# Kernel tuning notes

Hardware: AMD Instinct MI355X
Metric: run time of the kernel (lower is better)

## Reference

```python
import jax, jax.numpy as jnp
import numpy as np

B = 8          # number of subgraphs (seq_start_end rows)
N = 2048       # nodes per subgraph (equal-size segments)
D = 64         # h_dim
H = 4          # gat_heads
ALPHA = 0.2    # leaky relu slope


def setup_inputs() -> dict:
    key = jax.random.key(0)
    k1, k2, k3, k4, k5 = jax.random.split(key, 5)
    h_states = jax.random.normal(k1, (B * N, D), dtype=jnp.float32)
    # xavier-ish scales
    W_heads = jax.random.normal(k2, (H, D, D), dtype=jnp.float32) * (1.414 * np.sqrt(2.0 / (D + D)))
    a_heads = jax.random.normal(k3, (H, 2 * D), dtype=jnp.float32) * (1.414 * np.sqrt(2.0 / (2 * D + 1)))
    W_out = jax.random.normal(k4, (H * D, D), dtype=jnp.float32) * (1.414 * np.sqrt(2.0 / (H * D + D)))
    a_out = jax.random.normal(k5, (2 * D,), dtype=jnp.float32) * (1.414 * np.sqrt(2.0 / (2 * D + 1)))
    starts = jnp.arange(B, dtype=jnp.int32) * N
    seq_start_end = jnp.stack([starts, starts + N], axis=1)  # (B, 2)
    return {"h_states": h_states, "W_heads": W_heads, "a_heads": a_heads,
            "W_out": W_out, "a_out": a_out, "seq_start_end": seq_start_end}


def _gat_layer(x, W, a):
    """Dense GAT layer. Equivalent to the torch.cat O(N^2*2d) construction,
    rewritten as separate a1/a2 projections + broadcast add. Eval mode (no dropout)."""
    h = x @ W                      # (N, dout)
    d = W.shape[1]
    s1 = h @ a[:d]                 # (N,)  score contribution of source node i
    s2 = h @ a[d:]                 # (N,)  score contribution of target node j
    e = jax.nn.leaky_relu(s1[:, None] + s2[None, :], ALPHA)  # (N, N)
    attn = jax.nn.softmax(e, axis=1)
    return attn @ h                # (N, dout)


def reference(h_states, W_heads, a_heads, W_out, a_out, seq_start_end):
    # seq_start_end encodes B equal contiguous segments of length N -> reshape
    x = h_states.reshape(B, N, D)

    def per_graph(xg):  # xg: (N, D)
        # multi-head attention layers, concat=True -> elu on each head output
        hp = jax.vmap(lambda W, a: jax.nn.elu(_gat_layer(xg, W, a)))(W_heads, a_heads)  # (H, N, D)
        xc = jnp.transpose(hp, (1, 0, 2)).reshape(N, H * D)
        # output attention layer, concat=False (no elu inside), then elu + log_softmax outside
        out = jax.nn.elu(_gat_layer(xc, W_out, a_out))   # (N, D)
        return jax.nn.log_softmax(out, axis=1)

    return jax.vmap(per_graph)(x).reshape(B * N, D)
```

## Files before the change

kernel.cpp:

```cpp
#include <hip/hip_runtime.h>
#include <math.h>

#define NTOT 16384
#define NSEG 2048
#define TROW 65
#define TSTRIDE 133185ull

#define OFF_HH   0ull
#define OFF_XC   4194304ull
#define OFF_S1H  8388608ull
#define OFF_S2H  8454144ull
#define OFF_S1O  8519680ull
#define OFF_S2O  8536064ull
#define OFF_SVAL 8552448ull
#define OFF_WN   8617984ull
#define OFF_CHA  8683520ull
#define OFF_CHS  8949760ull
#define OFF_SIDX 9216000ull
#define OFF_A    9281536ull
#define OFF_S    13543456ull

__device__ inline unsigned long long pack_key(float v, int idx) {
    unsigned u = __float_as_uint(v);
    u = (u & 0x80000000u) ? ~u : (u | 0x80000000u);
    return ((unsigned long long)u << 32) | (unsigned)idx;
}
__device__ inline float unpack_key(unsigned long long k) {
    unsigned u = (unsigned)(k >> 32);
    u = (u & 0x80000000u) ? (u ^ 0x80000000u) : ~u;
    return __uint_as_float(u);
}
__device__ inline unsigned long long shfl_xor_u64(unsigned long long x, int mask) {
    unsigned lo = (unsigned)x, hi = (unsigned)(x >> 32);
    lo = (unsigned)__shfl_xor((int)lo, mask, 64);
    hi = (unsigned)__shfl_xor((int)hi, mask, 64);
    return ((unsigned long long)hi << 32) | lo;
}

__global__ __launch_bounds__(256) void gemm1_k(const float* __restrict__ X,
                                               const float* __restrict__ Wh,
                                               const float* __restrict__ aH,
                                               float* __restrict__ hh,
                                               float* __restrict__ s1h,
                                               float* __restrict__ s2h) {
    __shared__ float As[64][68];
    __shared__ float Bs[64][68];
    const int tid = threadIdx.x;
    const int bm = blockIdx.x, h = blockIdx.y;
    const int c0 = tid & 63, r0 = tid >> 6;
#pragma unroll
    for (int r = 0; r < 16; ++r) {
        int row = r0 + r * 4;
        As[c0][row] = X[(size_t)(bm * 64 + row) * 64 + c0];
        Bs[row][c0] = Wh[h * 4096 + row * 64 + c0];
    }
    __syncthreads();
    const int tx = tid & 15, ty = tid >> 4;
    const int m0 = ty * 4, n0 = tx * 4;
    float acc[4][4] = {};
#pragma unroll
    for (int kk = 0; kk < 64; ++kk) {
        float4 a = *(const float4*)&As[kk][m0];
        float4 b = *(const float4*)&Bs[kk][n0];
        acc[0][0] += a.x * b.x; acc[0][1] += a.x * b.y; acc[0][2] += a.x * b.z; acc[0][3] += a.x * b.w;
        acc[1][0] += a.y * b.x; acc[1][1] += a.y * b.y; acc[1][2] += a.y * b.z; acc[1][3] += a.y * b.w;
        acc[2][0] += a.z * b.x; acc[2][1] += a.z * b.y; acc[2][2] += a.z * b.z; acc[2][3] += a.z * b.w;
        acc[3][0] += a.w * b.x; acc[3][1] += a.w * b.y; acc[3][2] += a.w * b.z; acc[3][3] += a.w * b.w;
    }
#pragma unroll
    for (int i = 0; i < 4; ++i) {
        float4 v = make_float4(acc[i][0], acc[i][1], acc[i][2], acc[i][3]);
        *(float4*)&hh[(size_t)(bm * 64 + m0 + i) * 256 + h * 64 + n0] = v;
    }
#pragma unroll
    for (int i = 0; i < 4; ++i) {
        float p1 = 0.f, p2 = 0.f;
#pragma unroll
        for (int jj = 0; jj < 4; ++jj) {
            p1 += acc[i][jj] * aH[h * 128 + n0 + jj];
            p2 += acc[i][jj] * aH[h * 128 + 64 + n0 + jj];
        }
#pragma unroll
        for (int off = 8; off; off >>= 1) {
            p1 += __shfl_xor(p1, off, 16);
            p2 += __shfl_xor(p2, off, 16);
        }
        if (tx == 0) {
            s1h[h * NTOT + bm * 64 + m0 + i] = p1;
            s2h[h * NTOT + bm * 64 + m0 + i] = p2;
        }
    }
}

__global__ __launch_bounds__(256) void gemm2_k(const float* __restrict__ XC,
                                               const float* __restrict__ Wo,
                                               const float* __restrict__ aO,
                                               float* __restrict__ hc,
                                               float* __restrict__ s1o,
                                               float* __restrict__ s2o) {
    __shared__ float As[64][68];
    __shared__ float Bs[64][68];
    const int tid = threadIdx.x;
    const int bm = blockIdx.x;
    const int c0 = tid & 63, r0 = tid >> 6;
    const int tx = tid & 15, ty = tid >> 4;
    const int m0 = ty * 4, n0 = tx * 4;
    float acc[4][4] = {};
    for (int kt = 0; kt < 4; ++kt) {
#pragma unroll
        for (int r = 0; r < 16; ++r) {
            int row = r0 + r * 4;
            As[c0][row] = XC[(size_t)(bm * 64 + row) * 256 + kt * 64 + c0];
            Bs[row][c0] = Wo[(kt * 64 + row) * 64 + c0];
        }
        __syncthreads();
#pragma unroll
        for (int kk = 0; kk < 64; ++kk) {
            float4 a = *(const float4*)&As[kk][m0];
            float4 b = *(const float4*)&Bs[kk][n0];
            acc[0][0] += a.x * b.x; acc[0][1] += a.x * b.y; acc[0][2] += a.x * b.z; acc[0][3] += a.x * b.w;
            acc[1][0] += a.y * b.x; acc[1][1] += a.y * b.y; acc[1][2] += a.y * b.z; acc[1][3] += a.y * b.w;
            acc[2][0] += a.z * b.x; acc[2][1] += a.z * b.y; acc[2][2] += a.z * b.z; acc[2][3] += a.z * b.w;
            acc[3][0] += a.w * b.x; acc[3][1] += a.w * b.y; acc[3][2] += a.w * b.z; acc[3][3] += a.w * b.w;
        }
        __syncthreads();
    }
#pragma unroll
    for (int i = 0; i < 4; ++i) {
        float4 v = make_float4(acc[i][0], acc[i][1], acc[i][2], acc[i][3]);
        *(float4*)&hc[(size_t)(bm * 64 + m0 + i) * 64 + n0] = v;
    }
#pragma unroll
    for (int i = 0; i < 4; ++i) {
        float p1 = 0.f, p2 = 0.f;
#pragma unroll
        for (int jj = 0; jj < 4; ++jj) {
            p1 += acc[i][jj] * aO[n0 + jj];
            p2 += acc[i][jj] * aO[64 + n0 + jj];
        }
#pragma unroll
        for (int off = 8; off; off >>= 1) {
            p1 += __shfl_xor(p1, off, 16);
            p2 += __shfl_xor(p2, off, 16);
        }
        if (tx == 0) {
            s1o[bm * 64 + m0 + i] = p1;
            s2o[bm * 64 + m0 + i] = p2;
        }
    }
}

__global__ __launch_bounds__(1024) void sortchunkscan_k(const float* __restrict__ s2_all,
                                                        const float* __restrict__ V,
                                                        int heads, int vstride,
                                                        float* __restrict__ g_sval, int* __restrict__ g_sidx,
                                                        float* __restrict__ g_wN,
                                                        float* __restrict__ g_chA, float* __restrict__ g_chS,
                                                        float* __restrict__ g_A, float* __restrict__ g_S) {
    __shared__ unsigned long long sA[1024];
    __shared__ unsigned long long sB[1024];
    __shared__ float chA[8320];
    __shared__ float chS[8320];
    __shared__ float swn[NSEG];
    __shared__ int ssi[NSEG];
    __shared__ float btA[4][65];
    __shared__ float btS[4][65];
    __shared__ float sM2;
    const int tid = threadIdx.x, t = blockIdx.x;
    const int g = t / heads, h = t % heads;
    const float* s2p = s2_all + (size_t)h * NTOT + (size_t)g * NSEG;
    const float* Vp = V + (size_t)g * NSEG * vstride + h * 64;

    unsigned long long a0 = pack_key(s2p[tid], tid);
    unsigned long long a1 = pack_key(s2p[tid + 1024], tid + 1024);
    for (int k = 2; k <= 2048; k <<= 1) {
        const bool up0 = (tid & k) == 0;
        const bool up1 = (((tid + 1024) & k) == 0);
        for (int j = k >> 1; j > 0; j >>= 1) {
            if (j >= 1024) {
                unsigned long long lo = a0 < a1 ? a0 : a1;
                unsigned long long hi = a0 < a1 ? a1 : a0;
                a0 = up0 ? lo : hi;
                a1 = up0 ? hi : lo;
            } else if (j >= 64) {
                __syncthreads();
                sA[tid] = a0; sB[tid] = a1;
                __syncthreads();
                unsigned long long p0 = sA[tid ^ j], p1 = sB[tid ^ j];
                bool lower = (tid & j) == 0;
                a0 = ((a0 < p0) == (lower == up0)) ? a0 : p0;
                a1 = ((a1 < p1) == (lower == up1)) ? a1 : p1;
            } else {
                unsigned long long p0 = shfl_xor_u64(a0, j);
                unsigned long long p1 = shfl_xor_u64(a1, j);
                bool lower = (tid & j) == 0;
                a0 = ((a0 < p0) == (lower == up0)) ? a0 : p0;
                a1 = ((a1 < p1) == (lower == up1)) ? a1 : p1;
            }
        }
    }
    float v0 = unpack_key(a0), v1 = unpack_key(a1);
    if (tid == 1023) sM2 = v1;
    __syncthreads();
    const float M2 = sM2;
    int i0 = (int)(unsigned)(a0 & 0xffffffffu);
    int i1 = (int)(unsigned)(a1 & 0xffffffffu);
    float w0 = __expf(0.2f * (v0 - M2));
    float w1 = __expf(0.2f * (v1 - M2));
    size_t o = (size_t)t * NSEG;
    g_sval[o + tid] = v0; g_sval[o + tid + 1024] = v1;
    g_sidx[o + tid] = i0; g_sidx[o + tid + 1024] = i1;
    g_wN[o + tid] = w0;   g_wN[o + tid + 1024] = w1;
    swn[tid] = w0; swn[tid + 1024] = w1;
    ssi[tid] = i0; ssi[tid + 1024] = i1;
    __syncthreads();
    const int wv = tid >> 6, lane = tid & 63;
    for (int cc = 0; cc < 8; ++cc) {
        int c = wv * 8 + cc, base = c * 16;
        float sa = 0.f, swa = 0.f, ss = 0.f, sws = 0.f;
#pragma unroll
        for (int j = 0; j < 16; ++j) {
            float wn = swn[base + j];
            int row = ssi[base + j];
            float v = Vp[(size_t)row * vstride + lane];
            float w2 = wn * wn, wp = w2 * w2 * wn;
            sa += wn * v; swa += wn;
            ss += wp * v; sws += wp;
        }
        chA[c * 65 + lane] = sa; chS[c * 65 + lane] = ss;
        if (lane == 0) { chA[c * 65 + 64] = swa; chS[c * 65 + 64] = sws; }
    }
    __syncthreads();
    if (tid < 260) {
        int b = tid / 65, d = tid % 65;
        float run = 0.f;
        for (int c = b * 32; c < b * 32 + 32; ++c) { float v = chA[c * 65 + d]; chA[c * 65 + d] = run; run += v; }
        btA[b][d] = run;
    } else if (tid >= 512 && tid < 772) {
        int u = tid - 512;
        int b = u / 65, d = u % 65;
        float run = 0.f;
        for (int c = b * 32 + 31; c >= b * 32; --c) { run += chS[c * 65 + d]; chS[c * 65 + d] = run; }
        btS[b][d] = run;
    }
    __syncthreads();
    if (tid < 65) {
        float run = 0.f;
        for (int b = 0; b < 4; ++b) { float v = btA[b][tid]; btA[b][tid] = run; run += v; }
        g_A[(size_t)t * TSTRIDE + (size_t)2048 * TROW + tid] = run;
    } else if (tid >= 512 && tid < 577) {
        int d = tid - 512;
        float run = 0.f;
        for (int b = 3; b >= 0; --b) { float v = btS[b][d]; btS[b][d] = run; run += v; }
        g_S[(size_t)t * TSTRIDE + (size_t)2048 * TROW + d] = 0.f;
    }
    __syncthreads();
    if (tid < 512) {
        for (int i = tid; i < 8320; i += 512) chA[i] += btA[(i / 65) >> 5][i % 65];
    } else {
        for (int i = tid - 512; i < 8320; i += 512) chS[i] += btS[(i / 65) >> 5][i % 65];
    }
    __syncthreads();
    for (int i = tid; i < 8320; i += 1024) {
        g_chA[(size_t)t * 8320 + i] = chA[i];
        g_chS[(size_t)t * 8320 + i] = chS[i];
    }
}

__global__ __launch_bounds__(256) void seg_tab_k(const float* __restrict__ V,
                                                 int heads, int vstride,
                                                 const int* __restrict__ g_sidx,
                                                 const float* __restrict__ g_wN,
                                                 const float* __restrict__ g_chA,
                                                 const float* __restrict__ g_chS,
                                                 float* __restrict__ g_A, float* __restrict__ g_S) {
    const int t = blockIdx.y, g = t / heads, h = t % heads;
    const int wv = threadIdx.x >> 6, lane = threadIdx.x & 63;
    const int c = blockIdx.x * 4 + wv;
    const int base = c * 16;
    const float* Vp = V + (size_t)g * NSEG * vstride + h * 64;
    const int* sidx = g_sidx + (size_t)t * NSEG + base;
    const float* wnp = g_wN + (size_t)t * NSEG + base;
    float wn[16], vv[16];
#pragma unroll
    for (int j = 0; j < 16; ++j) wn[j] = wnp[j];
#pragma unroll
    for (int j = 0; j < 16; ++j) vv[j] = Vp[(size_t)sidx[j] * vstride + lane];
    float* A = g_A + (size_t)t * TSTRIDE;
    float* S = g_S + (size_t)t * TSTRIDE;
    float accA = g_chA[((size_t)t * 128 + c) * TROW + lane];
    float scaA = g_chA[((size_t)t * 128 + c) * TROW + 64];
#pragma unroll
    for (int j = 0; j < 16; ++j) {
        size_t pos = base + j;
        A[pos * TROW + lane] = accA;
        if (lane == 0) A[pos * TROW + 64] = scaA;
        accA += wn[j] * vv[j]; scaA += wn[j];
    }
    float accS = 0.f, scaS = 0.f;
    if (c < 127) {
        accS = g_chS[((size_t)t * 128 + c + 1) * TROW + lane];
        scaS = g_chS[((size_t)t * 128 + c + 1) * TROW + 64];
    }
#pragma unroll
    for (int j = 15; j >= 0; --j) {
        float w = wn[j], w2 = w * w, wp = w2 * w2 * w;
        accS += wp * vv[j]; scaS += wp;
        size_t pos = base + j;
        S[pos * TROW + lane] = accS;
        if (lane == 0) S[pos * TROW + 64] = scaS;
    }
}

template <int MODE>
__global__ __launch_bounds__(256) void seg_query_k(const float* __restrict__ s1_all,
                                                   float* __restrict__ out,
                                                   int heads, int ostride,
                                                   const float* __restrict__ g_sval,
                                                   const float* __restrict__ g_A,
                                                   const float* __restrict__ g_S) {
    __shared__ float sval[NSEG];
    const int tid = threadIdx.x;
    const int t = blockIdx.y, g = t / heads, h = t % heads;
    const float4* sv4 = (const float4*)(g_sval + (size_t)t * NSEG);
    for (int i = tid; i < NSEG / 4; i += 256) ((float4*)sval)[i] = sv4[i];
    __syncthreads();
    const float M2 = sval[NSEG - 1];
    const int lane = tid & 63, wv = tid >> 6;
    const int q0 = blockIdx.x * 64 + wv * 16;
    const float* s1p = s1_all + (size_t)h * NTOT + (size_t)g * NSEG;
    float* outp = out + (size_t)g * NSEG * ostride + h * 64;
    const float* A = g_A + (size_t)t * TSTRIDE;
    const float* S = g_S + (size_t)t * TSTRIDE;
    int myq = q0 + (lane & 15);
    float s1v = s1p[myq];
    float th = -s1v;
    int lo = 0, hi = NSEG;
    while (lo < hi) { int mid = (lo + hi) >> 1; if (sval[mid] <= th) lo = mid + 1; else hi = mid; }
    for (int j = 0; j < 16; ++j) {
        int k = __shfl(lo, j, 64);
        float s1q = __shfl(s1v, j, 64);
        const float* rowA = A + (size_t)k * TROW;
        const float* rowS = S + (size_t)k * TROW;
        float accA = rowA[lane], scaA = rowA[64];
        float accS = rowS[lane], scaS = rowS[64];
        float cc = __expf(-0.8f * fmaxf(s1q + M2, 0.f));
        float o = (accS + cc * accA) / (scaS + cc * scaA);
        o = o > 0.f ? o : expm1f(o);
        int q = q0 + j;
        if (MODE == 0) {
            outp[(size_t)q * ostride + lane] = o;
        } else {
            float m = o;
#pragma unroll
            for (int off = 32; off; off >>= 1) m = fmaxf(m, __shfl_xor(m, off, 64));
            float e = __expf(o - m);
#pragma unroll
            for (int off = 32; off; off >>= 1) e += __shfl_xor(e, off, 64);
            outp[(size_t)q * ostride + lane] = o - m - __logf(e);
        }
    }
}

extern "C" void kernel_launch(void* const* d_in, const int* in_sizes, int n_in,
                              void* d_out, int out_size, void* d_ws, size_t ws_size,
                              hipStream_t stream) {
    const float* h_states = (const float*)d_in[0];
    const float* W_heads = (const float*)d_in[1];
    const float* a_heads = (const float*)d_in[2];
    const float* W_out = (const float*)d_in[3];
    const float* a_out = (const float*)d_in[4];
    float* w = (float*)d_ws;
    float* hh = w + OFF_HH;
    float* xc = w + OFF_XC;
    float* hc = w + OFF_HH;
    float* s1h = w + OFF_S1H;
    float* s2h = w + OFF_S2H;
    float* s1o = w + OFF_S1O;
    float* s2o = w + OFF_S2O;
    float* g_sval = w + OFF_SVAL;
    float* g_wN = w + OFF_WN;
    float* g_chA = w + OFF_CHA;
    float* g_chS = w + OFF_CHS;
    int* g_sidx = (int*)(w + OFF_SIDX);
    float* g_A = w + OFF_A;
    float* g_S = w + OFF_S;
    float* outp = (float*)d_out;

    gemm1_k<<<dim3(256, 4), 256, 0, stream>>>(h_states, W_heads, a_heads, hh, s1h, s2h);
    sortchunkscan_k<<<32, 1024, 0, stream>>>(s2h, hh, 4, 256, g_sval, g_sidx, g_wN, g_chA, g_chS, g_A, g_S);
    seg_tab_k<<<dim3(32, 32), 256, 0, stream>>>(hh, 4, 256, g_sidx, g_wN, g_chA, g_chS, g_A, g_S);
    seg_query_k<0><<<dim3(32, 32), 256, 0, stream>>>(s1h, xc, 4, 256, g_sval, g_A, g_S);
    gemm2_k<<<256, 256, 0, stream>>>(xc, W_out, a_out, hc, s1o, s2o);
    sortchunkscan_k<<<8, 1024, 0, stream>>>(s2o, hc, 1, 64, g_sval, g_sidx, g_wN, g_chA, g_chS, g_A, g_S);
    seg_tab_k<<<dim3(32, 8), 256, 0, stream>>>(hc, 1, 64, g_sidx, g_wN, g_chA, g_chS, g_A, g_S);
    seg_query_k<1><<<dim3(32, 8), 256, 0, stream>>>(s1o, outp, 1, 64, g_sval, g_A, g_S);
}
```

Before: 203.6 us.

## Split sort from chunk scan and apply chunk prefixes at query time

The sort kernel no longer gathers V rows or computes chunk totals; it only sorts and writes sorted values, indices and weights. The table kernel now builds local within-chunk prefix and suffix sums plus per-chunk totals. A small new scan kernel computes the chunk-level exclusive prefixes, and the query kernel adds them when reading table rows. The bitonic sort also double-buffers its shared arrays to drop one barrier per step. This removes the heavy serial gather-and-scan from a 32-block kernel, at the cost of an extra launch and extra loads per query.

```diff
diff --git a/kernel.cpp b/kernel.cpp
--- a/kernel.cpp
+++ b/kernel.cpp
@@ -4,7 +4,8 @@
 #define NTOT 16384
 #define NSEG 2048
 #define TROW 65
-#define TSTRIDE 133185ull
+#define TSTRIDE 133120ull
+#define CSTRIDE 8385ull
 
 #define OFF_HH   0ull
 #define OFF_XC   4194304ull
@@ -14,11 +15,11 @@
 #define OFF_S2O  8536064ull
 #define OFF_SVAL 8552448ull
 #define OFF_WN   8617984ull
-#define OFF_CHA  8683520ull
-#define OFF_CHS  8949760ull
-#define OFF_SIDX 9216000ull
-#define OFF_A    9281536ull
-#define OFF_S    13543456ull
+#define OFF_SIDX 8683520ull
+#define OFF_CA   8749056ull
+#define OFF_CS   9017376ull
+#define OFF_A    9285696ull
+#define OFF_S    13545536ull
 
 __device__ inline unsigned long long pack_key(float v, int idx) {
     unsigned u = __float_as_uint(v);
@@ -150,29 +151,21 @@
     }
 }
 
-__global__ __launch_bounds__(1024) void sortchunkscan_k(const float* __restrict__ s2_all,
-                                                        const float* __restrict__ V,
-                                                        int heads, int vstride,
-                                                        float* __restrict__ g_sval, int* __restrict__ g_sidx,
-                                                        float* __restrict__ g_wN,
-                                                        float* __restrict__ g_chA, float* __restrict__ g_chS,
-                                                        float* __restrict__ g_A, float* __restrict__ g_S) {
-    __shared__ unsigned long long sA[1024];
-    __shared__ unsigned long long sB[1024];
-    __shared__ float chA[8320];
-    __shared__ float chS[8320];
-    __shared__ float swn[NSEG];
-    __shared__ int ssi[NSEG];
-    __shared__ float btA[4][65];
-    __shared__ float btS[4][65];
+__global__ __launch_bounds__(1024) void sort_k(const float* __restrict__ s2_all,
+                                               int heads,
+                                               float* __restrict__ g_sval,
+                                               int* __restrict__ g_sidx,
+                                               float* __restrict__ g_wN) {
+    __shared__ unsigned long long sA[2][1024];
+    __shared__ unsigned long long sB[2][1024];
     __shared__ float sM2;
     const int tid = threadIdx.x, t = blockIdx.x;
     const int g = t / heads, h = t % heads;
     const float* s2p = s2_all + (size_t)h * NTOT + (size_t)g * NSEG;
-    const float* Vp = V + (size_t)g * NSEG * vstride + h * 64;
 
     unsigned long long a0 = pack_key(s2p[tid], tid);
     unsigned long long a1 = pack_key(s2p[tid + 1024], tid + 1024);
+    int p = 0;
     for (int k = 2; k <= 2048; k <<= 1) {
         const bool up0 = (tid & k) == 0;
         const bool up1 = (((tid + 1024) & k) == 0);
@@ -183,19 +176,19 @@
                 a0 = up0 ? lo : hi;
                 a1 = up0 ? hi : lo;
             } else if (j >= 64) {
+                sA[p][tid] = a0; sB[p][tid] = a1;
                 __syncthreads();
-                sA[tid] = a0; sB[tid] = a1;
-                __syncthreads();
-                unsigned long long p0 = sA[tid ^ j], p1 = sB[tid ^ j];
+                unsigned long long q0 = sA[p][tid ^ j], q1 = sB[p][tid ^ j];
                 bool lower = (tid & j) == 0;
-                a0 = ((a0 < p0) == (lower == up0)) ? a0 : p0;
-                a1 = ((a1 < p1) == (lower == up1)) ? a1 : p1;
+                a0 = ((a0 < q0) == (lower == up0)) ? a0 : q0;
+                a1 = ((a1 < q1) == (lower == up1)) ? a1 : q1;
+                p ^= 1;
             } else {
-                unsigned long long p0 = shfl_xor_u64(a0, j);
-                unsigned long long p1 = shfl_xor_u64(a1, j);
+                unsigned long long q0 = shfl_xor_u64(a0, j);
+                unsigned long long q1 = shfl_xor_u64(a1, j);
                 bool lower = (tid & j) == 0;
-                a0 = ((a0 < p0) == (lower == up0)) ? a0 : p0;
-                a1 = ((a1 < p1) == (lower == up1)) ? a1 : p1;
+                a0 = ((a0 < q0) == (lower == up0)) ? a0 : q0;
+                a1 = ((a1 < q1) == (lower == up1)) ? a1 : q1;
             }
         }
     }
@@ -211,69 +204,14 @@
     g_sval[o + tid] = v0; g_sval[o + tid + 1024] = v1;
     g_sidx[o + tid] = i0; g_sidx[o + tid + 1024] = i1;
     g_wN[o + tid] = w0;   g_wN[o + tid + 1024] = w1;
-    swn[tid] = w0; swn[tid + 1024] = w1;
-    ssi[tid] = i0; ssi[tid + 1024] = i1;
-    __syncthreads();
-    const int wv = tid >> 6, lane = tid & 63;
-    for (int cc = 0; cc < 8; ++cc) {
-        int c = wv * 8 + cc, base = c * 16;
-        float sa = 0.f, swa = 0.f, ss = 0.f, sws = 0.f;
-#pragma unroll
-        for (int j = 0; j < 16; ++j) {
-            float wn = swn[base + j];
-            int row = ssi[base + j];
-            float v = Vp[(size_t)row * vstride + lane];
-            float w2 = wn * wn, wp = w2 * w2 * wn;
-            sa += wn * v; swa += wn;
-            ss += wp * v; sws += wp;
-        }
-        chA[c * 65 + lane] = sa; chS[c * 65 + lane] = ss;
-        if (lane == 0) { chA[c * 65 + 64] = swa; chS[c * 65 + 64] = sws; }
-    }
-    __syncthreads();
-    if (tid < 260) {
-        int b = tid / 65, d = tid % 65;
-        float run = 0.f;
-        for (int c = b * 32; c < b * 32 + 32; ++c) { float v = chA[c * 65 + d]; chA[c * 65 + d] = run; run += v; }
-        btA[b][d] = run;
-    } else if (tid >= 512 && tid < 772) {
-        int u = tid - 512;
-        int b = u / 65, d = u % 65;
-        float run = 0.f;
-        for (int c = b * 32 + 31; c >= b * 32; --c) { run += chS[c * 65 + d]; chS[c * 65 + d] = run; }
-        btS[b][d] = run;
-    }
-    __syncthreads();
-    if (tid < 65) {
-        float run = 0.f;
-        for (int b = 0; b < 4; ++b) { float v = btA[b][tid]; btA[b][tid] = run; run += v; }
-        g_A[(size_t)t * TSTRIDE + (size_t)2048 * TROW + tid] = run;
-    } else if (tid >= 512 && tid < 577) {
-        int d = tid - 512;
-        float run = 0.f;
-        for (int b = 3; b >= 0; --b) { float v = btS[b][d]; btS[b][d] = run; run += v; }
-        g_S[(size_t)t * TSTRIDE + (size_t)2048 * TROW + d] = 0.f;
-    }
-    __syncthreads();
-    if (tid < 512) {
-        for (int i = tid; i < 8320; i += 512) chA[i] += btA[(i / 65) >> 5][i % 65];
-    } else {
-        for (int i = tid - 512; i < 8320; i += 512) chS[i] += btS[(i / 65) >> 5][i % 65];
-    }
-    __syncthreads();
-    for (int i = tid; i < 8320; i += 1024) {
-        g_chA[(size_t)t * 8320 + i] = chA[i];
-        g_chS[(size_t)t * 8320 + i] = chS[i];
-    }
-}
-
-__global__ __launch_bounds__(256) void seg_tab_k(const float* __restrict__ V,
-                                                 int heads, int vstride,
-                                                 const int* __restrict__ g_sidx,
-                                                 const float* __restrict__ g_wN,
-                                                 const float* __restrict__ g_chA,
-                                                 const float* __restrict__ g_chS,
-                                                 float* __restrict__ g_A, float* __restrict__ g_S) {
+}
+
+__global__ __launch_bounds__(256) void tabw_k(const float* __restrict__ V,
+                                              int heads, int vstride,
+                                              const int* __restrict__ g_sidx,
+                                              const float* __restrict__ g_wN,
+                                              float* __restrict__ g_A, float* __restrict__ g_S,
+                                              float* __restrict__ g_TA, float* __restrict__ g_TS) {
     const int t = blockIdx.y, g = t / heads, h = t % heads;
     const int wv = threadIdx.x >> 6, lane = threadIdx.x & 63;
     const int c = blockIdx.x * 4 + wv;
@@ -288,8 +226,7 @@
     for (int j = 0; j < 16; ++j) vv[j] = Vp[(size_t)sidx[j] * vstride + lane];
     float* A = g_A + (size_t)t * TSTRIDE;
     float* S = g_S + (size_t)t * TSTRIDE;
-    float accA = g_chA[((size_t)t * 128 + c) * TROW + lane];
-    float scaA = g_chA[((size_t)t * 128 + c) * TROW + 64];
+    float accA = 0.f, scaA = 0.f;
 #pragma unroll
     for (int j = 0; j < 16; ++j) {
         size_t pos = base + j;
@@ -297,11 +234,9 @@
         if (lane == 0) A[pos * TROW + 64] = scaA;
         accA += wn[j] * vv[j]; scaA += wn[j];
     }
+    g_TA[((size_t)t * 128 + c) * TROW + lane] = accA;
+    if (lane == 0) g_TA[((size_t)t * 128 + c) * TROW + 64] = scaA;
     float accS = 0.f, scaS = 0.f;
-    if (c < 127) {
-        accS = g_chS[((size_t)t * 128 + c + 1) * TROW + lane];
-        scaS = g_chS[((size_t)t * 128 + c + 1) * TROW + 64];
-    }
 #pragma unroll
     for (int j = 15; j >= 0; --j) {
         float w = wn[j], w2 = w * w, wp = w2 * w2 * w;
@@ -310,15 +245,41 @@
         S[pos * TROW + lane] = accS;
         if (lane == 0) S[pos * TROW + 64] = scaS;
     }
+    g_TS[((size_t)t * 128 + c) * TROW + lane] = accS;
+    if (lane == 0) g_TS[((size_t)t * 128 + c) * TROW + 64] = scaS;
+}
+
+__global__ __launch_bounds__(256) void scan_k(const float* __restrict__ g_TA,
+                                              const float* __restrict__ g_TS,
+                                              float* __restrict__ g_CA,
+                                              float* __restrict__ g_CS) {
+    const int t = blockIdx.x, tid = threadIdx.x;
+    if (tid < 65) {
+        const float* TA = g_TA + (size_t)t * 128 * TROW + tid;
+        float* CA = g_CA + (size_t)t * CSTRIDE + tid;
+        float run = 0.f;
+#pragma unroll 4
+        for (int c = 0; c < 128; ++c) { CA[c * TROW] = run; run += TA[c * TROW]; }
+        CA[128 * TROW] = run;
+    } else if (tid >= 128 && tid < 193) {
+        const int d = tid - 128;
+        const float* TS = g_TS + (size_t)t * 128 * TROW + d;
+        float* CS = g_CS + (size_t)t * CSTRIDE + d;
+        float run = 0.f;
+#pragma unroll 4
+        for (int c = 127; c >= 0; --c) { CS[c * TROW] = run; run += TS[c * TROW]; }
+    }
 }
 
 template <int MODE>
-__global__ __launch_bounds__(256) void seg_query_k(const float* __restrict__ s1_all,
-                                                   float* __restrict__ out,
-                                                   int heads, int ostride,
-                                                   const float* __restrict__ g_sval,
-                                                   const float* __restrict__ g_A,
-                                                   const float* __restrict__ g_S) {
+__global__ __launch_bounds__(256) void query_k(const float* __restrict__ s1_all,
+                                               float* __restrict__ out,
+                                               int heads, int ostride,
+                                               const float* __restrict__ g_sval,
+                                               const float* __restrict__ g_A,
+                                               const float* __restrict__ g_S,
+                                               const float* __restrict__ g_CA,
+                                               const float* __restrict__ g_CS) {
     __shared__ float sval[NSEG];
     const int tid = threadIdx.x;
     const int t = blockIdx.y, g = t / heads, h = t % heads;
@@ -332,6 +293,8 @@
     float* outp = out + (size_t)g * NSEG * ostride + h * 64;
     const float* A = g_A + (size_t)t * TSTRIDE;
     const float* S = g_S + (size_t)t * TSTRIDE;
+    const float* CA = g_CA + (size_t)t * CSTRIDE;
+    const float* CS = g_CS + (size_t)t * CSTRIDE;
     int myq = q0 + (lane & 15);
     float s1v = s1p[myq];
     float th = -s1v;
@@ -340,10 +303,19 @@
     for (int j = 0; j < 16; ++j) {
         int k = __shfl(lo, j, 64);
         float s1q = __shfl(s1v, j, 64);
-        const float* rowA = A + (size_t)k * TROW;
-        const float* rowS = S + (size_t)k * TROW;
-        float accA = rowA[lane], scaA = rowA[64];
-        float accS = rowS[lane], scaS = rowS[64];
+        float accA, scaA, accS, scaS;
+        if (k < NSEG) {
+            const int c = k >> 4;
+            const float* rowA = A + (size_t)k * TROW;
+            const float* rowS = S + (size_t)k * TROW;
+            const float* rowCA = CA + (size_t)c * TROW;
+            const float* rowCS = CS + (size_t)c * TROW;
+            accA = rowA[lane] + rowCA[lane]; scaA = rowA[64] + rowCA[64];
+            accS = rowS[lane] + rowCS[lane]; scaS = rowS[64] + rowCS[64];
+        } else {
+            accA = CA[128 * TROW + lane]; scaA = CA[128 * TROW + 64];
+            accS = 0.f; scaS = 0.f;
+        }
         float cc = __expf(-0.8f * fmaxf(s1q + M2, 0.f));
         float o = (accS + cc * accA) / (scaS + cc * scaA);
         o = o > 0.f ? o : expm1f(o);
@@ -380,19 +352,23 @@
     float* s2o = w + OFF_S2O;
     float* g_sval = w + OFF_SVAL;
     float* g_wN = w + OFF_WN;
-    float* g_chA = w + OFF_CHA;
-    float* g_chS = w + OFF_CHS;
     int* g_sidx = (int*)(w + OFF_SIDX);
+    float* g_TA = w + OFF_XC;
+    float* g_TS = w + OFF_XC + 266240;
+    float* g_CA = w + OFF_CA;
+    float* g_CS = w + OFF_CS;
     float* g_A = w + OFF_A;
     float* g_S = w + OFF_S;
     float* outp = (float*)d_out;
 
     gemm1_k<<<dim3(256, 4), 256, 0, stream>>>(h_states, W_heads, a_heads, hh, s1h, s2h);
-    sortchunkscan_k<<<32, 1024, 0, stream>>>(s2h, hh, 4, 256, g_sval, g_sidx, g_wN, g_chA, g_chS, g_A, g_S);
-    seg_tab_k<<<dim3(32, 32), 256, 0, stream>>>(hh, 4, 256, g_sidx, g_wN, g_chA, g_chS, g_A, g_S);
-    seg_query_k<0><<<dim3(32, 32), 256, 0, stream>>>(s1h, xc, 4, 256, g_sval, g_A, g_S);
+    sort_k<<<32, 1024, 0, stream>>>(s2h, 4, g_sval, g_sidx, g_wN);
+    tabw_k<<<dim3(32, 32), 256, 0, stream>>>(hh, 4, 256, g_sidx, g_wN, g_A, g_S, g_TA, g_TS);
+    scan_k<<<32, 256, 0, stream>>>(g_TA, g_TS, g_CA, g_CS);
+    query_k<0><<<dim3(32, 32), 256, 0, stream>>>(s1h, xc, 4, 256, g_sval, g_A, g_S, g_CA, g_CS);
     gemm2_k<<<256, 256, 0, stream>>>(xc, W_out, a_out, hc, s1o, s2o);
-    sortchunkscan_k<<<8, 1024, 0, stream>>>(s2o, hc, 1, 64, g_sval, g_sidx, g_wN, g_chA, g_chS, g_A, g_S);
-    seg_tab_k<<<dim3(32, 8), 256, 0, stream>>>(hc, 1, 64, g_sidx, g_wN, g_chA, g_chS, g_A, g_S);
-    seg_query_k<1><<<dim3(32, 8), 256, 0, stream>>>(s1o, outp, 1, 64, g_sval, g_A, g_S);
-}
+    sort_k<<<8, 1024, 0, stream>>>(s2o, 1, g_sval, g_sidx, g_wN);
+    tabw_k<<<dim3(32, 8), 256, 0, stream>>>(hc, 1, 64, g_sidx, g_wN, g_A, g_S, g_TA, g_TS);
+    scan_k<<<8, 256, 0, stream>>>(g_TA, g_TS, g_CA, g_CS);
+    query_k<1><<<dim3(32, 8), 256, 0, stream>>>(s1o, outp, 1, 64, g_sval, g_A, g_S, g_CA, g_CS);
+}
```

After: 200.3 us. Within noise of the previous version (-1.6%).
